# Kernel optimization log

Hardware: AMD Instinct MI355X
Metric: run time of the kernel (lower is better)

## Reference

```python
import jax, jax.numpy as jnp
import numpy as np

NUM_HEADS = 8
KEY_DIM = 32      # head_dim * attention_ratio = 64 * 0.5
HEAD_DIM = 64     # in_channels // num_heads = 512 // 8
SCALE = KEY_DIM ** -0.5


def _bn(y, g, b):
    # eval-mode BatchNorm2d with running_mean=0, running_var=1 -> per-channel affine
    return y * g[:, None, None] + b[:, None, None]


def setup_inputs() -> dict:
    key = jax.random.key(0)
    ks = jax.random.split(key, 4)
    B, C, H, W = 16, 512, 32, 32
    qkv_ch = C + 2 * NUM_HEADS * KEY_DIM  # 1024
    return {
        "x": jax.random.normal(ks[0], (B, C, H, W), jnp.float32),
        "w_qkv": jax.random.normal(ks[1], (qkv_ch, C), jnp.float32) * 0.02,
        "g_qkv": jnp.ones((qkv_ch,), jnp.float32),
        "b_qkv": jnp.zeros((qkv_ch,), jnp.float32),
        "w_pos": jax.random.normal(ks[2], (C, 1, 3, 3), jnp.float32) * 0.1,
        "g_pos": jnp.ones((C,), jnp.float32),
        "b_pos": jnp.zeros((C,), jnp.float32),
        "w_out": jax.random.normal(ks[3], (C, C), jnp.float32) * 0.02,
        "g_out": jnp.ones((C,), jnp.float32),
        "b_out": jnp.zeros((C,), jnp.float32),
    }


def reference(x, w_qkv, g_qkv, b_qkv, w_pos, g_pos, b_pos, w_out, g_out, b_out):
    B, C, H, W = x.shape
    HW = H * W
    # 1x1 conv QKV projection + BN (no activation)
    qkv = _bn(jnp.einsum('bchw,oc->bohw', x, w_qkv), g_qkv, b_qkv)
    # b (heads * (2*kd + hd)) h w -> b heads (2*kd + hd) hw
    qkv = qkv.reshape(B, NUM_HEADS, 2 * KEY_DIM + HEAD_DIM, HW)
    q = qkv[:, :, :KEY_DIM]                      # [B, h, kd, HW]
    k = qkv[:, :, KEY_DIM:2 * KEY_DIM]           # [B, h, kd, HW]
    v = qkv[:, :, 2 * KEY_DIM:]                  # [B, h, hd, HW]
    # attention scores: q^T k, scaled
    scores = jnp.einsum('bhdn,bhdm->bhnm', q, k) * SCALE   # [B, h, HW, HW]
    weights = jax.nn.softmax(scores, axis=-1)
    # attended = v @ weights^T : [B, h, hd, HW]
    attended = jnp.einsum('bhdm,bhnm->bhdn', v, weights)
    attended = attended.reshape(B, C, H, W)
    # positional encoding: depthwise 3x3 conv on value, + BN
    v_spatial = v.reshape(B, C, H, W)
    pos = jax.lax.conv_general_dilated(
        v_spatial, w_pos, window_strides=(1, 1), padding='SAME',
        feature_group_count=C, dimension_numbers=('NCHW', 'OIHW', 'NCHW'))
    pos = _bn(pos, g_pos, b_pos)
    enhanced = attended + pos
    # 1x1 output projection + BN
    return _bn(jnp.einsum('bchw,oc->bohw', enhanced, w_out), g_out, b_out)
```

## Files before the change

### kernel.cpp

```cpp
#include <hip/hip_runtime.h>
#include <hip/hip_bf16.h>
#include <stdint.h>

#define NHEADS 8
#define KDIM   32
#define HDIM   64
#define CDIM   512
#define HWN    1024
#define BATCH  16
#define QKVCH  1024
#define SCALE_F 0.17677669529663687f
#define QSCALE_F (0.17677669529663687f * 1.44269504088896341f)

typedef __attribute__((ext_vector_type(8))) short short8;
typedef __attribute__((ext_vector_type(4))) float f32x4;

static __device__ __forceinline__ unsigned short f2bf(float f) {
    unsigned int u = __float_as_uint(f);
    unsigned int r = (u + 0x7fffu + ((u >> 16) & 1u)) >> 16;
    return (unsigned short)r;
}
static __device__ __forceinline__ float bf2f(unsigned short h) {
    return __uint_as_float(((unsigned int)h) << 16);
}
static __device__ __forceinline__ unsigned int cvtpk(float a, float b) {
    unsigned int r;
    asm("v_cvt_pk_bf16_f32 %0, %1, %2" : "=v"(r) : "v"(a), "v"(b));
    return r;
}
static __device__ __forceinline__ float fexp2(float x) {
    float r;
    asm("v_exp_f32 %0, %1" : "=v"(r) : "v"(x));
    return r;
}
static __device__ __forceinline__ float bfelem(const uint4& v, int j) {
    unsigned int w = ((j >> 1) == 0) ? v.x : ((j >> 1) == 1) ? v.y : ((j >> 1) == 2) ? v.z : v.w;
    return (j & 1) ? __uint_as_float(w & 0xffff0000u) : __uint_as_float(w << 16);
}
static __device__ __forceinline__ unsigned int addpk(unsigned int a, unsigned int p) {
    float lo = __uint_as_float(a << 16) + __uint_as_float(p << 16);
    float hi = __uint_as_float(a & 0xffff0000u) + __uint_as_float(p & 0xffff0000u);
    return cvtpk(lo, hi);
}

static __device__ __forceinline__ void gload_lds16(const void* g, void* l) {
    __builtin_amdgcn_global_load_lds(
        (const __attribute__((address_space(1))) void*)g,
        (__attribute__((address_space(3))) void*)l, 16, 0, 0);
}

__global__ __launch_bounds__(256) void convert_kernel(const float* __restrict__ src,
                                                      unsigned short* __restrict__ dst, int n) {
    int i = (blockIdx.x * 256 + threadIdx.x) * 8;
    if (i >= n) return;
    float4 a = *(const float4*)(src + i);
    float4 c = *(const float4*)(src + i + 4);
    unsigned short r[8] __attribute__((aligned(16))) =
        {f2bf(a.x), f2bf(a.y), f2bf(a.z), f2bf(a.w), f2bf(c.x), f2bf(c.y), f2bf(c.z), f2bf(c.w)};
    *(uint4*)(dst + i) = *(const uint4*)r;
}

__global__ __launch_bounds__(256) void transpose_kernel(const float* __restrict__ x,
                                                        unsigned short* __restrict__ xt) {
    __shared__ unsigned short tl[64][66];
    int bid = blockIdx.x;
    int b = bid >> 7, ct = (bid >> 4) & 7, nt = bid & 15;
    int t = threadIdx.x;
#pragma unroll
    for (int i = 0; i < 16; ++i) {
        int idx = i * 256 + t;
        int cl = idx >> 6, nl = idx & 63;
        tl[cl][nl] = f2bf(x[((size_t)(b * CDIM + ct * 64 + cl)) * HWN + nt * 64 + nl]);
    }
    __syncthreads();
    int a8 = (t & 7) * 8;
    int nl = t >> 3;
#pragma unroll
    for (int i = 0; i < 2; ++i) {
        int n = nt * 64 + nl + 32 * i;
        unsigned short tmp[8] __attribute__((aligned(16)));
#pragma unroll
        for (int j = 0; j < 8; ++j) tmp[j] = tl[a8 + j][nl + 32 * i];
        *(uint4*)(xt + ((size_t)b * HWN + n) * CDIM + ct * 64 + a8) = *(const uint4*)tmp;
    }
}

template <int MODE, int BN, int WM, int WN, int NTB>
__global__ __launch_bounds__(512, 2) void gemm_bf16(
    const unsigned short* __restrict__ A, const unsigned short* __restrict__ Bt,
    const float* __restrict__ gvec, const float* __restrict__ bvec,
    void* out0, void* out1, void* out2) {
    constexpr int MF = 256 / (16 * WM);
    constexpr int NF = BN / (16 * WN);
    constexpr int BUFE = (256 + BN) * 64;
    constexpr int BUNITS = BN * 8 / 512;
    constexpr int PHB = BN * 4;
    __shared__ unsigned short lds[2][BUFE];

    int p = blockIdx.x;
    int xcd = p & 7;
    int j2 = p >> 3;
    int b = xcd * 2 + (j2 >= 16 ? 1 : 0);
    int idx = j2 & 15;
    int mt = idx / NTB, ntl = idx % NTB;
    int t = threadIdx.x, lane = t & 63, w = t >> 6, g = lane >> 4, lr = lane & 15;
    int M0 = mt * 256, N0 = ntl * BN;
    int wr = (w / WN) * (16 * MF), wc = (w % WN) * (16 * NF);

    const unsigned short* Ab = A + (size_t)M0 * 512;
    const unsigned short* Bb = Bt + (size_t)b * HWN * 512 + (size_t)N0 * 512;

    auto stage = [&](int kt, int buf) {
        unsigned short* base = &lds[buf][0];
#pragma unroll
        for (int i = 0; i < 4; ++i) {
            int U0 = i * 512 + w * 64;
            int U = U0 + lane;
            int h = U >> 10, rem = U & 1023;
            int row = ((rem >> 6) << 4) + (lane & 15);
            int k = ((lane >> 4) << 3) + (h << 5);
            gload_lds16(Ab + (size_t)row * 512 + kt * 64 + k, (char*)base + U0 * 16);
        }
#pragma unroll
        for (int i = 0; i < BUNITS; ++i) {
            int U0 = i * 512 + w * 64;
            int U = U0 + lane;
            int h = U / PHB, rem = U % PHB;
            int row = ((rem >> 6) << 4) + (lane & 15);
            int k = ((lane >> 4) << 3) + (h << 5);
            gload_lds16(Bb + (size_t)row * 512 + kt * 64 + k, (char*)base + 32768 + U0 * 16);
        }
    };

    f32x4 acc[MF][NF] = {};
    stage(0, 0);
    __syncthreads();
    for (int kt = 0; kt < 8; ++kt) {
        int cur = kt & 1;
        if (kt < 7) stage(kt + 1, cur ^ 1);
        const unsigned short* base = &lds[cur][0];
#pragma unroll
        for (int h = 0; h < 2; ++h) {
            short8 af[MF], bfr[NF];
#pragma unroll
            for (int i = 0; i < MF; ++i)
                af[i] = *(const short8*)(base + h * 8192 + (((wr >> 4) + i) * 64 + lane) * 8);
#pragma unroll
            for (int j = 0; j < NF; ++j)
                bfr[j] = *(const short8*)(base + 16384 + h * (BN * 32) + (((wc >> 4) + j) * 64 + lane) * 8);
#pragma unroll
            for (int i = 0; i < MF; ++i)
#pragma unroll
                for (int j = 0; j < NF; ++j)
                    acc[i][j] = __builtin_amdgcn_mfma_f32_16x16x32_bf16(af[i], bfr[j], acc[i][j], 0, 0, 0);
        }
        __syncthreads();
    }

#pragma unroll
    for (int i = 0; i < MF; ++i) {
        int obase = M0 + wr + i * 16 + g * 4;
#pragma unroll
        for (int j = 0; j < NF; ++j) {
            int n = N0 + wc + j * 16 + lr;
            float val[4];
#pragma unroll
            for (int rr = 0; rr < 4; ++rr) {
                int o = obase + rr;
                val[rr] = acc[i][j][rr] * gvec[o] + bvec[o];
            }
            if (MODE == 0) {
                int h = obase >> 7, jj = obase & 127;
                size_t bh = (size_t)((b << 3) + h);
                if (jj < 32) {
                    uint2 pk = {cvtpk(val[0] * QSCALE_F, val[1] * QSCALE_F),
                                cvtpk(val[2] * QSCALE_F, val[3] * QSCALE_F)};
                    *(uint2*)((unsigned short*)out0 + (bh * HWN + n) * KDIM + jj) = pk;
                } else if (jj < 64) {
                    uint2 pk = {cvtpk(val[0], val[1]), cvtpk(val[2], val[3])};
                    *(uint2*)((unsigned short*)out1 + (bh * HWN + n) * KDIM + (jj - 32)) = pk;
                } else {
#pragma unroll
                    for (int rr = 0; rr < 4; ++rr)
                        ((unsigned short*)out2)[(bh * HDIM + (jj - 64 + rr)) * HWN + n] = f2bf(val[rr]);
                }
            } else {
#pragma unroll
                for (int rr = 0; rr < 4; ++rr)
                    ((float*)out0)[((size_t)(b * CDIM + obase + rr)) * HWN + n] = val[rr];
            }
        }
    }
}

__global__ __launch_bounds__(256) void attn_kernel(
    const unsigned short* __restrict__ qw, const unsigned short* __restrict__ kw,
    const unsigned short* __restrict__ vw, unsigned short* __restrict__ attw) {
    __shared__ unsigned short kt[2][128 * 32];
    __shared__ unsigned short vt[2][64 * 128];
    int p = blockIdx.x;
    int bh = ((p >> 6) << 3) | (p & 7);
    int ntile = (p >> 3) & 7;
    int b = bh >> 3, h = bh & 7;
    int t = threadIdx.x, lane = t & 63, w = t >> 6, g = lane >> 4, lr = lane & 15;
    int N0 = ntile * 128 + w * 32;
    const unsigned short* qb = qw + (size_t)bh * HWN * KDIM;
    const unsigned short* kb = kw + (size_t)bh * HWN * KDIM;
    const unsigned short* vb = vw + (size_t)bh * HDIM * HWN;

    short8 qf0 = *(const short8*)(qb + (size_t)(N0 + lr) * KDIM + g * 8);
    short8 qf1 = *(const short8*)(qb + (size_t)(N0 + 16 + lr) * KDIM + g * 8);
    f32x4 acc0[4] = {}, acc1[4] = {};
    f32x4 zero = {0.f, 0.f, 0.f, 0.f};
    float l0 = 0.f, l1 = 0.f;
    int sw = (lr & 7) << 4;
    int g8 = g << 3;

    auto stage = [&](int mt, int buf) {
        int M0 = mt * 128;
#pragma unroll
        for (int pp = 0; pp < 2; ++pp) {
            int s = pp * 256 + w * 64 + lane;
            int row = (s >> 7) * 32 + ((s >> 6) & 1) * 16 + lr;
            gload_lds16(kb + (size_t)(M0 + row) * KDIM + g * 8,
                        (char*)kt[buf] + (pp * 4 + w) * 1024);
        }
#pragma unroll
        for (int pp = 0; pp < 4; ++pp) {
            int s = pp * 256 + w * 64 + lane;
            int dd = s >> 4, u = s & 15;
            gload_lds16(vb + (size_t)dd * HWN + M0 + ((u ^ (dd & 7)) << 3),
                        (char*)vt[buf] + (pp * 4 + w) * 1024);
        }
    };

    stage(0, 0);
    __syncthreads();
    for (int mt = 0; mt < 8; ++mt) {
        int cur = mt & 1;
        if (mt < 7) stage(mt + 1, cur ^ 1);
        const char* ktc = (const char*)kt[cur] + lane * 16;
        const char* vrow = (const char*)vt[cur] + lr * 256;
#pragma unroll
        for (int mc = 0; mc < 4; ++mc) {
            short8 kf0 = *(const short8*)(ktc + mc * 2048);
            short8 kf1 = *(const short8*)(ktc + mc * 2048 + 1024);
            f32x4 s00 = __builtin_amdgcn_mfma_f32_16x16x32_bf16(kf0, qf0, zero, 0, 0, 0);
            f32x4 s01 = __builtin_amdgcn_mfma_f32_16x16x32_bf16(kf1, qf0, zero, 0, 0, 0);
            f32x4 s10 = __builtin_amdgcn_mfma_f32_16x16x32_bf16(kf0, qf1, zero, 0, 0, 0);
            f32x4 s11 = __builtin_amdgcn_mfma_f32_16x16x32_bf16(kf1, qf1, zero, 0, 0, 0);
            float e0[8], e1[8];
#pragma unroll
            for (int i = 0; i < 4; ++i) {
                e0[i] = fexp2(s00[i]); e0[4 + i] = fexp2(s01[i]);
                e1[i] = fexp2(s10[i]); e1[4 + i] = fexp2(s11[i]);
            }
            l0 += ((e0[0] + e0[1]) + (e0[2] + e0[3])) + ((e0[4] + e0[5]) + (e0[6] + e0[7]));
            l1 += ((e1[0] + e1[1]) + (e1[2] + e1[3])) + ((e1[4] + e1[5]) + (e1[6] + e1[7]));
            union { uint4 u; short8 s; } pf0, pf1;
            pf0.u = (uint4){cvtpk(e0[0], e0[1]), cvtpk(e0[2], e0[3]),
                            cvtpk(e0[4], e0[5]), cvtpk(e0[6], e0[7])};
            pf1.u = (uint4){cvtpk(e1[0], e1[1]), cvtpk(e1[2], e1[3]),
                            cvtpk(e1[4], e1[5]), cvtpk(e1[6], e1[7])};
            int off0 = (mc * 64 + g8) ^ sw;
            int off1 = off0 ^ 32;
#pragma unroll
            for (int dt = 0; dt < 4; ++dt) {
                uint2 v0 = *(const uint2*)(vrow + dt * 4096 + off0);
                uint2 v1 = *(const uint2*)(vrow + dt * 4096 + off1);
                union { uint2 u[2]; short8 s; } vf;
                vf.u[0] = v0; vf.u[1] = v1;
                acc0[dt] = __builtin_amdgcn_mfma_f32_16x16x32_bf16(vf.s, pf0.s, acc0[dt], 0, 0, 0);
                acc1[dt] = __builtin_amdgcn_mfma_f32_16x16x32_bf16(vf.s, pf1.s, acc1[dt], 0, 0, 0);
            }
        }
        __syncthreads();
    }
    l0 += __shfl_xor(l0, 16); l0 += __shfl_xor(l0, 32);
    l1 += __shfl_xor(l1, 16); l1 += __shfl_xor(l1, 32);
    float inv0 = 1.0f / l0, inv1 = 1.0f / l1;
    size_t robase = ((size_t)b * HWN + N0 + lr) * CDIM + h * HDIM + g * 4;
#pragma unroll
    for (int dt = 0; dt < 4; ++dt) {
        uint2 o0 = {cvtpk(acc0[dt][0] * inv0, acc0[dt][1] * inv0),
                    cvtpk(acc0[dt][2] * inv0, acc0[dt][3] * inv0)};
        uint2 o1 = {cvtpk(acc1[dt][0] * inv1, acc1[dt][1] * inv1),
                    cvtpk(acc1[dt][2] * inv1, acc1[dt][3] * inv1)};
        *(uint2*)(attw + robase + dt * 16) = o0;
        *(uint2*)(attw + robase + 16 * CDIM + dt * 16) = o1;
    }
}

__global__ __launch_bounds__(256) void conv_kernel(
    const unsigned short* __restrict__ vw,
    const float* __restrict__ wpos, const float* __restrict__ gpos, const float* __restrict__ bpos,
    const unsigned short* __restrict__ attw,
    unsigned short* __restrict__ ew) {
    __shared__ unsigned short po[32][520];
    int bid = blockIdx.x;
    int b = bid >> 5, y = bid & 31;
    int t = threadIdx.x;
#pragma unroll
    for (int hh = 0; hh < 2; ++hh) {
        int c = hh * 256 + t;
        const unsigned short* vrow = vw + ((size_t)(b * CDIM + c)) * HWN;
        uint4 rv[3][4];
#pragma unroll
        for (int dy = 0; dy < 3; ++dy) {
            int r = y + dy - 1;
            bool ok = (r >= 0) && (r < 32);
#pragma unroll
            for (int s2 = 0; s2 < 4; ++s2) {
                uint4 z = {0u, 0u, 0u, 0u};
                rv[dy][s2] = ok ? *(const uint4*)(vrow + r * 32 + s2 * 8) : z;
            }
        }
        float wreg[9];
#pragma unroll
        for (int k = 0; k < 9; ++k) wreg[k] = wpos[c * 9 + k];
        float gc = gpos[c], bc = bpos[c];
#pragma unroll
        for (int x = 0; x < 32; ++x) {
            float sum = 0.f;
#pragma unroll
            for (int dy = 0; dy < 3; ++dy)
#pragma unroll
                for (int dx = 0; dx < 3; ++dx) {
                    int xx = x + dx - 1;
                    if (xx >= 0 && xx < 32)
                        sum += wreg[dy * 3 + dx] * bfelem(rv[dy][xx >> 3], xx & 7);
                }
            po[x][c] = f2bf(sum * gc + bc);
        }
    }
    __syncthreads();
    int c8 = (t & 63) * 8;
    int xg = t >> 6;
#pragma unroll
    for (int i = 0; i < 8; ++i) {
        int x = xg + i * 4;
        size_t nidx = ((size_t)b * HWN + y * 32 + x) * CDIM + c8;
        uint4 a = *(const uint4*)(attw + nidx);
        uint4 p = *(const uint4*)(&po[x][c8]);
        uint4 o = {addpk(a.x, p.x), addpk(a.y, p.y), addpk(a.z, p.z), addpk(a.w, p.w)};
        *(uint4*)(ew + nidx) = o;
    }
}

extern "C" void kernel_launch(void* const* d_in, const int* in_sizes, int n_in,
                              void* d_out, int out_size, void* d_ws, size_t ws_size,
                              hipStream_t stream) {
    const float* x     = (const float*)d_in[0];
    const float* w_qkv = (const float*)d_in[1];
    const float* g_qkv = (const float*)d_in[2];
    const float* b_qkv = (const float*)d_in[3];
    const float* w_pos = (const float*)d_in[4];
    const float* g_pos = (const float*)d_in[5];
    const float* b_pos = (const float*)d_in[6];
    const float* w_out = (const float*)d_in[7];
    const float* g_out = (const float*)d_in[8];
    const float* b_out = (const float*)d_in[9];
    char* ws = (char*)d_ws;
    unsigned short* xt   = (unsigned short*)(ws);
    unsigned short* wqb  = (unsigned short*)(ws + 16777216);
    unsigned short* wob  = (unsigned short*)(ws + 17825792);
    unsigned short* qw   = (unsigned short*)(ws + 18350080);
    unsigned short* kw   = (unsigned short*)(ws + 26738688);
    unsigned short* vw   = (unsigned short*)(ws + 35127296);
    unsigned short* attw = (unsigned short*)(ws + 51904512);

    convert_kernel<<<256, 256, 0, stream>>>(w_qkv, wqb, QKVCH * CDIM);
    convert_kernel<<<128, 256, 0, stream>>>(w_out, wob, CDIM * CDIM);
    transpose_kernel<<<2048, 256, 0, stream>>>(x, xt);
    gemm_bf16<0, 256, 2, 4, 4><<<256, 512, 0, stream>>>(wqb, xt, g_qkv, b_qkv, qw, kw, vw);
    attn_kernel<<<1024, 256, 0, stream>>>(qw, kw, vw, attw);
    conv_kernel<<<512, 256, 0, stream>>>(vw, w_pos, g_pos, b_pos, attw, xt );
    gemm_bf16<1, 128, 4, 2, 8><<<256, 512, 0, stream>>>(wob, xt , g_out, b_out, d_out, nullptr, nullptr);
}
```

Measured before the change: 141.7 us.

## Split GEMM prefetch into A/B halves interleaved with MFMA; XCD-aware conv block mapping

The GEMM kernel's next-tile prefetch is split into separate A and B staging calls, each issued just before one half-K of MFMA work, so global-to-LDS loads are spread across the compute instead of all issued at once. The conv kernel remaps block indices so that blocks on the same XCD handle the same batch images, matching the GEMM's XCD mapping for better L2 locality of the attention output and V reads. The interleaving relies on each half's LDS region not being read by the in-flight MFMAs of the same buffer. It may also change how the compiler schedules instructions and uses registers.

```diff
diff --git a/kernel.cpp b/kernel.cpp
--- a/kernel.cpp
+++ b/kernel.cpp
@@ -110,7 +110,7 @@
     const unsigned short* Ab = A + (size_t)M0 * 512;
     const unsigned short* Bb = Bt + (size_t)b * HWN * 512 + (size_t)N0 * 512;
 
-    auto stage = [&](int kt, int buf) {
+    auto stage_a = [&](int kt, int buf) {
         unsigned short* base = &lds[buf][0];
 #pragma unroll
         for (int i = 0; i < 4; ++i) {
@@ -121,6 +121,9 @@
             int k = ((lane >> 4) << 3) + (h << 5);
             gload_lds16(Ab + (size_t)row * 512 + kt * 64 + k, (char*)base + U0 * 16);
         }
+    };
+    auto stage_b = [&](int kt, int buf) {
+        unsigned short* base = &lds[buf][0];
 #pragma unroll
         for (int i = 0; i < BUNITS; ++i) {
             int U0 = i * 512 + w * 64;
@@ -133,21 +136,36 @@
     };
 
     f32x4 acc[MF][NF] = {};
-    stage(0, 0);
+    stage_a(0, 0);
+    stage_b(0, 0);
     __syncthreads();
     for (int kt = 0; kt < 8; ++kt) {
         int cur = kt & 1;
-        if (kt < 7) stage(kt + 1, cur ^ 1);
         const unsigned short* base = &lds[cur][0];
-#pragma unroll
-        for (int h = 0; h < 2; ++h) {
+        if (kt < 7) stage_a(kt + 1, cur ^ 1);
+        {
             short8 af[MF], bfr[NF];
 #pragma unroll
             for (int i = 0; i < MF; ++i)
-                af[i] = *(const short8*)(base + h * 8192 + (((wr >> 4) + i) * 64 + lane) * 8);
+                af[i] = *(const short8*)(base + (((wr >> 4) + i) * 64 + lane) * 8);
 #pragma unroll
             for (int j = 0; j < NF; ++j)
-                bfr[j] = *(const short8*)(base + 16384 + h * (BN * 32) + (((wc >> 4) + j) * 64 + lane) * 8);
+                bfr[j] = *(const short8*)(base + 16384 + (((wc >> 4) + j) * 64 + lane) * 8);
+#pragma unroll
+            for (int i = 0; i < MF; ++i)
+#pragma unroll
+                for (int j = 0; j < NF; ++j)
+                    acc[i][j] = __builtin_amdgcn_mfma_f32_16x16x32_bf16(af[i], bfr[j], acc[i][j], 0, 0, 0);
+        }
+        if (kt < 7) stage_b(kt + 1, cur ^ 1);
+        {
+            short8 af[MF], bfr[NF];
+#pragma unroll
+            for (int i = 0; i < MF; ++i)
+                af[i] = *(const short8*)(base + 8192 + (((wr >> 4) + i) * 64 + lane) * 8);
+#pragma unroll
+            for (int j = 0; j < NF; ++j)
+                bfr[j] = *(const short8*)(base + 16384 + BN * 32 + (((wc >> 4) + j) * 64 + lane) * 8);
 #pragma unroll
             for (int i = 0; i < MF; ++i)
 #pragma unroll
@@ -297,8 +315,10 @@
     const unsigned short* __restrict__ attw,
     unsigned short* __restrict__ ew) {
     __shared__ unsigned short po[32][520];
-    int bid = blockIdx.x;
-    int b = bid >> 5, y = bid & 31;
+    int p = blockIdx.x;
+    int xcd = p & 7, q = p >> 3;
+    int b = xcd * 2 + (q >> 5);
+    int y = q & 31;
     int t = threadIdx.x;
 #pragma unroll
     for (int hh = 0; hh < 2; ++hh) {
@@ -341,8 +361,8 @@
         int x = xg + i * 4;
         size_t nidx = ((size_t)b * HWN + y * 32 + x) * CDIM + c8;
         uint4 a = *(const uint4*)(attw + nidx);
-        uint4 p = *(const uint4*)(&po[x][c8]);
-        uint4 o = {addpk(a.x, p.x), addpk(a.y, p.y), addpk(a.z, p.z), addpk(a.w, p.w)};
+        uint4 pp = *(const uint4*)(&po[x][c8]);
+        uint4 o = {addpk(a.x, pp.x), addpk(a.y, pp.y), addpk(a.z, pp.z), addpk(a.w, pp.w)};
         *(uint4*)(ew + nidx) = o;
     }
 }
```

Result: faster. 138.5 us (-2.2%).
